# Kernel optimization log

Hardware: AMD Instinct MI355X
Metric: run time of the kernel (lower is better)

The kernel has to match this reference:

```python
import jax, jax.numpy as jnp
import numpy as np

HIS = 10   # history steps (node_feature_dim = 10*4)
ROLL = 2   # args.pred_roll
MP = 2     # message_passing_steps
N = 20000  # num nodes (balls)
E = 320000 # num edges


def _mlp(x, W1, b1, W2, b2, g, be):
    # two-layer ELU MLP + BatchNorm1d (training mode: batch statistics)
    h = jax.nn.elu(x @ W1 + b1)
    h = jax.nn.elu(h @ W2 + b2)
    B, M, C = h.shape
    f = h.reshape(B * M, C)
    mu = f.mean(0)
    var = ((f - mu) ** 2).mean(0)  # biased variance, as torch BN training
    f = (f - mu) * jax.lax.rsqrt(var + 1e-5) * g + be
    return f.reshape(B, M, C)


def setup_inputs() -> dict:
    key = jax.random.key(0)
    ks = jax.random.split(key, 16)

    def lin(k, i, o):
        W = jax.random.normal(k, (i, o), jnp.float32) / jnp.sqrt(jnp.float32(i))
        b = jnp.full((o,), 0.1, jnp.float32)
        return W, b

    inp = {}
    inp["nodes"] = jax.random.normal(ks[0], (1, HIS + ROLL, N, 4), jnp.float32)
    inp["edge_pair"] = jax.random.randint(ks[1], (E, 2), 0, N)
    inp["edge_attr"] = jax.random.normal(ks[2], (E, 2), jnp.float32)
    # encoder node MLP: 40 -> 128 -> 128
    inp["en_W1"], inp["en_b1"] = lin(ks[3], 40, 128)
    inp["en_W2"], inp["en_b2"] = lin(ks[4], 128, 128)
    inp["en_g"], inp["en_be"] = jnp.ones((128,), jnp.float32), jnp.zeros((128,), jnp.float32)
    # encoder edge MLP: 6 -> 32 -> 32
    inp["ee_W1"], inp["ee_b1"] = lin(ks[5], 6, 32)
    inp["ee_W2"], inp["ee_b2"] = lin(ks[6], 32, 32)
    inp["ee_g"], inp["ee_be"] = jnp.ones((32,), jnp.float32), jnp.zeros((32,), jnp.float32)
    # GraphNetBlock edge MLP: 288 -> 128 -> 32
    inp["ge_W1"], inp["ge_b1"] = lin(ks[7], 288, 128)
    inp["ge_W2"], inp["ge_b2"] = lin(ks[8], 128, 32)
    inp["ge_g"], inp["ge_be"] = jnp.ones((32,), jnp.float32), jnp.zeros((32,), jnp.float32)
    # GraphNetBlock node MLP: 160 -> 256 -> 128
    inp["gn_W1"], inp["gn_b1"] = lin(ks[9], 160, 256)
    inp["gn_W2"], inp["gn_b2"] = lin(ks[10], 256, 128)
    inp["gn_g"], inp["gn_be"] = jnp.ones((128,), jnp.float32), jnp.zeros((128,), jnp.float32)
    # decoder: Linear(128,128) Tanh Linear(128,2)
    inp["d_W1"], inp["d_b1"] = lin(ks[11], 128, 128)
    inp["d_W2"], inp["d_b2"] = lin(ks[12], 128, 2)
    return inp


def _forward(nodes, edge_pair, edge_attr,
             en_W1, en_b1, en_W2, en_b2, en_g, en_be,
             ee_W1, ee_b1, ee_W2, ee_b2, ee_g, ee_be,
             ge_W1, ge_b1, ge_W2, ge_b2, ge_g, ge_be,
             gn_W1, gn_b1, gn_W2, gn_b2, gn_g, gn_be,
             d_W1, d_b1, d_W2, d_b2):
    window = nodes[0]                 # [T, N, 4]
    n = window.shape[1]
    s0 = edge_pair[:, 0]
    s1 = edge_pair[:, 1]
    # history features: [1, N, HIS*4]
    history = jnp.transpose(window[:HIS], (1, 0, 2)).reshape(1, n, -1)
    gt_future = window[HIS:]          # [ROLL, N, 4]
    # initial edge features: raw 2-dim attr + |pos/vel diff| (4-dim) -> 6
    pd0 = jnp.abs(window[HIS][s0] - window[HIS][s1])   # [E, 4]
    edge_feat = jnp.concatenate([edge_attr[None], pd0[None]], -1)  # [1, E, 6]
    cur_pos = window[HIS - 1, :, :2]
    cur_vel = window[HIS - 1, :, 2:]
    preds = []
    for _ in range(ROLL):
        ln = _mlp(history, en_W1, en_b1, en_W2, en_b2, en_g, en_be)    # [1,N,128]
        le = _mlp(edge_feat, ee_W1, ee_b1, ee_W2, ee_b2, ee_g, ee_be)  # [1,E,32]
        for _ in range(MP):
            # edge update: gather sender/receiver, MLP
            ef = jnp.concatenate([ln[:, s0], ln[:, s1], le], -1)       # [1,E,288]
            ne = _mlp(ef, ge_W1, ge_b1, ge_W2, ge_b2, ge_g, ge_be)     # [1,E,32]
            # node aggregation: scatter-add at both endpoints
            agg = jnp.zeros((n, ne.shape[-1]), ne.dtype)
            agg = agg.at[s0].add(ne[0]).at[s1].add(ne[0])
            nf = jnp.concatenate([ln, agg[None]], -1)                  # [1,N,160]
            nn_ = _mlp(nf, gn_W1, gn_b1, gn_W2, gn_b2, gn_g, gn_be)
            ln = nn_ + ln
            le = ne + le
        accel = jnp.tanh(ln @ d_W1 + d_b1) @ d_W2 + d_b2               # [1,N,2]
        prev_pos = cur_pos
        cur_pos = 2 * cur_pos + accel - prev_pos                       # [1,N,2]
        cur_vel = cur_vel + accel
        pd = jnp.abs(cur_pos[:, s0] - cur_pos[:, s1])                  # [1,E,2]
        edge_feat = edge_feat.at[:, :, -2:].set(pd)
        preds.append(cur_pos)
        hist4 = history.reshape(1, n, HIS, 4)
        new_state = jnp.concatenate([cur_pos.reshape(1, n, 1, 2),
                                     cur_vel.reshape(1, n, 1, 2)], -1)
        history = jnp.concatenate([hist4[:, :, 1:, :], new_state], -2).reshape(1, n, -1)
    preds = jnp.stack(preds, 1)                                        # [1,ROLL,N,2]
    diff = preds[0] - gt_future[:, :, :2]
    variance = 5e-5
    loss_nll = (diff ** 2 / (2 * variance)).sum() / (ROLL * n)
    loss_mse = (diff ** 2).mean()
    return preds, loss_nll, loss_mse, gt_future


def reference(nodes, edge_pair, edge_attr,
              en_W1, en_b1, en_W2, en_b2, en_g, en_be,
              ee_W1, ee_b1, ee_W2, ee_b2, ee_g, ee_be,
              ge_W1, ge_b1, ge_W2, ge_b2, ge_g, ge_be,
              gn_W1, gn_b1, gn_W2, gn_b2, gn_g, gn_be,
              d_W1, d_b1, d_W2, d_b2):
    return _forward(nodes, edge_pair, edge_attr,
                    en_W1, en_b1, en_W2, en_b2, en_g, en_be,
                    ee_W1, ee_b1, ee_W2, ee_b2, ee_g, ee_be,
                    ge_W1, ge_b1, ge_W2, ge_b2, ge_g, ge_be,
                    gn_W1, gn_b1, gn_W2, gn_b2, gn_g, gn_be,
                    d_W1, d_b1, d_W2, d_b2)
```

## Files before the change

kernel.cpp:

```cpp
#include <hip/hip_runtime.h>


constexpr int NN = 20000;
constexpr int NE = 320000;
constexpr int NSLOT = 32;
constexpr int SSTR = 512;

typedef __attribute__((ext_vector_type(8))) short short8;
typedef __attribute__((ext_vector_type(4))) float f32x4;

__device__ __forceinline__ float act_elu(float x) { return x > 0.f ? x : __expf(x) - 1.f; }
__device__ __forceinline__ unsigned short f2bf(float f) {
  unsigned u = __builtin_bit_cast(unsigned, f);
  return (unsigned short)((u + 0x7FFFu + ((u >> 16) & 1u)) >> 16);
}
__device__ __forceinline__ float bf2f(unsigned short h) {
  unsigned u = ((unsigned)h) << 16; return __builtin_bit_cast(float, u);
}
__device__ __forceinline__ void atomic_pk_bf16(unsigned short* addr, float a, float b) {
  unsigned v = (unsigned)f2bf(a) | ((unsigned)f2bf(b) << 16);
  asm volatile("global_atomic_pk_add_bf16 %0, %1, off"
               :: "v"(addr), "v"(v) : "memory");
}

template<int K1, int K1P, int C1, int C2, int BM, int NWM, int NWC, int NWM2, int NWC2,
         int ACT2, bool STATS, int MODE>
__global__ __launch_bounds__(256) void mlp2_k(
    const unsigned short* __restrict__ A,
    const unsigned short* __restrict__ Wt1, const float* __restrict__ b1,
    const unsigned short* __restrict__ Wt2, const float* __restrict__ b2,
    unsigned short* __restrict__ out, int M, float* __restrict__ stat,
    unsigned short* __restrict__ aggB, const float* __restrict__ statP, float invE,
    const float* __restrict__ gg, const float* __restrict__ gb,
    float* __restrict__ sclW, const int* __restrict__ dg0, const int* __restrict__ dg1)
{
  constexpr int FM  = BM / (16 * NWM);
  constexpr int FC  = C1 / (16 * NWC);
  constexpr int FM2 = BM / (16 * NWM2);
  constexpr int FC2 = C2 / (16 * NWC2);
  constexpr int NKS1 = K1P / 32;
  constexpr int NKS2 = C1 / 32;
  constexpr int AST = K1P + 8;
  constexpr int P1 = C1 + 8;
  constexpr int P2 = C2 + 8;
  constexpr int ACH = K1P / 8;
  static_assert(NWM * NWC == 4 && NWM2 * NWC2 == 4, "4 waves");
  static_assert(C2 <= C1, "repack reuses H1");

  __shared__ unsigned short As[BM * AST];
  __shared__ unsigned short H1[BM * P1];
  __shared__ float red[2][C2];
  __shared__ float s_scl[(MODE == 4) ? 32 : 1], s_shf[(MODE == 4) ? 32 : 1];

  const int tid = threadIdx.x;
  const int row0 = blockIdx.x * BM;
  const int wave = tid >> 6, lane = tid & 63;
  const int wm = wave % NWM, wc = wave / NWM;
  const int wm2 = wave % NWM2, wc2 = wave / NWM2;
  const int lr = lane & 15, kg = lane >> 4;

  if (STATS) for (int i = tid; i < 2 * C2; i += 256) ((float*)red)[i] = 0.f;

  if constexpr (MODE == 4) {
    if (tid < 32) {
      float su = 0.f, sq = 0.f;
      for (int s = 0; s < NSLOT; ++s) {
        su += statP[(size_t)s * SSTR + tid];
        sq += statP[(size_t)s * SSTR + 256 + tid];
      }
      float mu = su * invE;
      float var = sq * invE - mu * mu;
      float sc = rsqrtf(var + 1e-5f) * gg[tid];
      float sh = gb[tid] - mu * sc;
      s_scl[tid] = sc; s_shf[tid] = sh;
      if (blockIdx.x == 0) { sclW[tid] = sc; sclW[32 + tid] = sh; }
    }
    __syncthreads();
  }

  for (int idx = tid; idx < BM * ACH; idx += 256) {
    int m = idx / ACH, chk = idx % ACH;
    int kglob = chk * 8;
    int row = row0 + m;
    uint4 v = make_uint4(0, 0, 0, 0);
    if (row < M) {
      if constexpr (MODE == 0) {
        if (kglob + 8 <= K1) v = *(const uint4*)(A + (size_t)row * K1 + kglob);
      } else if constexpr (MODE == 3) {
        if (chk == 0) v = *(const uint4*)(A + (size_t)row * 8);
      } else {
        if (kglob < 128) {
          v = *(const uint4*)(A + (size_t)row * 128 + kglob);
        } else {
          int c0 = kglob - 128;
          unsigned short* ap = &aggB[(size_t)row * 32 + c0];
          uint4 av4 = *(uint4*)ap;
          *(uint4*)ap = make_uint4(0, 0, 0, 0);
          const unsigned short* avp = (const unsigned short*)&av4;
          float d = (float)(dg0[row] + dg1[row]);
          unsigned short* vp = (unsigned short*)&v;
#pragma unroll
          for (int j = 0; j < 8; ++j)
            vp[j] = f2bf(fmaf(s_scl[c0 + j], bf2f(avp[j]), d * s_shf[c0 + j]));
        }
      }
    }
    *(uint4*)&As[m * AST + chk * 8] = v;
  }
  __syncthreads();

  f32x4 acc1[FM][FC];
#pragma unroll
  for (int i = 0; i < FM; ++i)
#pragma unroll
    for (int j = 0; j < FC; ++j) acc1[i][j] = (f32x4){0.f, 0.f, 0.f, 0.f};

#pragma unroll
  for (int ks = 0; ks < NKS1; ++ks) {
    const int k0 = ks * 32;
    short8 af[FM], bfr[FC];
#pragma unroll
    for (int i = 0; i < FM; ++i) {
      int r = (wm * FM + i) * 16 + lr;
      af[i] = __builtin_bit_cast(short8, *(const uint4*)&As[r * AST + k0 + kg * 8]);
    }
#pragma unroll
    for (int j = 0; j < FC; ++j) {
      int c = (wc * FC + j) * 16 + lr;
      bfr[j] = __builtin_bit_cast(short8, *(const uint4*)&Wt1[(size_t)c * K1P + k0 + kg * 8]);
    }
#pragma unroll
    for (int i = 0; i < FM; ++i)
#pragma unroll
      for (int j = 0; j < FC; ++j)
        acc1[i][j] = __builtin_amdgcn_mfma_f32_16x16x32_bf16(af[i], bfr[j], acc1[i][j], 0, 0, 0);
  }

  {
    float bl1[FC];
#pragma unroll
    for (int j = 0; j < FC; ++j) bl1[j] = b1[(wc * FC + j) * 16 + lr];
#pragma unroll
    for (int i = 0; i < FM; ++i)
#pragma unroll
      for (int t = 0; t < 4; ++t) {
        int rl = (wm * FM + i) * 16 + kg * 4 + t;
#pragma unroll
        for (int j = 0; j < FC; ++j)
          H1[rl * P1 + (wc * FC + j) * 16 + lr] = f2bf(act_elu(acc1[i][j][t] + bl1[j]));
      }
  }
  __syncthreads();

  f32x4 acc2[FM2][FC2];
#pragma unroll
  for (int i = 0; i < FM2; ++i)
#pragma unroll
    for (int j = 0; j < FC2; ++j) acc2[i][j] = (f32x4){0.f, 0.f, 0.f, 0.f};

#pragma unroll
  for (int ks = 0; ks < NKS2; ++ks) {
    const int k0 = ks * 32;
    short8 af[FM2], bfr[FC2];
#pragma unroll
    for (int i = 0; i < FM2; ++i) {
      int r = (wm2 * FM2 + i) * 16 + lr;
      af[i] = __builtin_bit_cast(short8, *(const uint4*)&H1[r * P1 + k0 + kg * 8]);
    }
#pragma unroll
    for (int j = 0; j < FC2; ++j) {
      int c = (wc2 * FC2 + j) * 16 + lr;
      bfr[j] = __builtin_bit_cast(short8, *(const uint4*)&Wt2[(size_t)c * C1 + k0 + kg * 8]);
    }
#pragma unroll
    for (int i = 0; i < FM2; ++i)
#pragma unroll
      for (int j = 0; j < FC2; ++j)
        acc2[i][j] = __builtin_amdgcn_mfma_f32_16x16x32_bf16(af[i], bfr[j], acc2[i][j], 0, 0, 0);
  }
  __syncthreads();

  float psum[FC2], psq[FC2], bl2[FC2];
#pragma unroll
  for (int j = 0; j < FC2; ++j) {
    psum[j] = 0.f; psq[j] = 0.f;
    bl2[j] = b2[(wc2 * FC2 + j) * 16 + lr];
  }
#pragma unroll
  for (int i = 0; i < FM2; ++i)
#pragma unroll
    for (int t = 0; t < 4; ++t) {
      int rl = (wm2 * FM2 + i) * 16 + kg * 4 + t;
      bool ok = (row0 + rl) < M;
#pragma unroll
      for (int j = 0; j < FC2; ++j) {
        float v = acc2[i][j][t] + bl2[j];
        if (ACT2 == 1) v = act_elu(v);
        else if (ACT2 == 2) v = tanhf(v);
        if (STATS && ok) { psum[j] += v; psq[j] += v * v; }
        H1[rl * P2 + (wc2 * FC2 + j) * 16 + lr] = f2bf(v);
      }
    }
  if (STATS) {
#pragma unroll
    for (int j = 0; j < FC2; ++j) {
      int c = (wc2 * FC2 + j) * 16 + lr;
      atomicAdd(&red[0][c], psum[j]);
      atomicAdd(&red[1][c], psq[j]);
    }
  }
  __syncthreads();
  for (int idx = tid; idx < BM * (C2 / 8); idx += 256) {
    int r = idx / (C2 / 8), cc = idx % (C2 / 8);
    int row = row0 + r;
    if (row < M)
      *(uint4*)&out[(size_t)row * C2 + cc * 8] = *(const uint4*)&H1[r * P2 + cc * 8];
  }
  if (STATS) {
    float* st = stat + (size_t)(blockIdx.x & (NSLOT - 1)) * SSTR;
    for (int i = tid; i < C2; i += 256) {
      atomicAdd(&st[i], red[0][i]);
      atomicAdd(&st[256 + i], red[1][i]);
    }
  }
}

template<int K, int C, int BM, int NWM, int NWC, int ACT, int DEC, int BNST>
__global__ __launch_bounds__(256) void mgemm_k(
    const unsigned short* __restrict__ Ah2,
    unsigned short* __restrict__ Aln,
    const unsigned short* __restrict__ Wt, const float* __restrict__ bias,
    unsigned short* __restrict__ out, int M,
    const float* __restrict__ statP, float invN,
    const float* __restrict__ gv, const float* __restrict__ bev,
    const float* __restrict__ pubStat, const float* __restrict__ pubG,
    const float* __restrict__ pubBe, float invPub, float* __restrict__ pubW,
    const float* __restrict__ W2f, const float* __restrict__ b2f,
    float* __restrict__ pos, float* __restrict__ vel, float* __restrict__ preds)
{
  constexpr int FM = BM / (16 * NWM);
  constexpr int FC = C / (16 * NWC);
  constexpr int NKS = K / 32;
  constexpr int AST = K + 8;
  constexpr int P2 = C + 8;
  constexpr int ACH = K / 8;
  static_assert(NWM * NWC == 4, "4 waves");
  static_assert(BNST == 0 || K == 128, "BN staging assumes K=128");

  __shared__ unsigned short As[BM * AST];
  __shared__ unsigned short Ob[BM * P2];
  __shared__ float Wl[DEC ? 256 : 1];
  __shared__ float s_scl[BNST ? 128 : 1], s_shf[BNST ? 128 : 1];

  const int tid = threadIdx.x;
  const int row0 = blockIdx.x * BM;
  const int wave = tid >> 6, lane = tid & 63;
  const int wm = wave % NWM, wc = wave / NWM;
  const int lr = lane & 15, kg = lane >> 4;

  if constexpr (BNST > 0) {
    if (tid < 128) {
      float su = 0.f, sq = 0.f;
      for (int s = 0; s < NSLOT; ++s) {
        su += statP[(size_t)s * SSTR + tid];
        sq += statP[(size_t)s * SSTR + 256 + tid];
      }
      float mu = su * invN;
      float var = sq * invN - mu * mu;
      float sc = rsqrtf(var + 1e-5f) * gv[tid];
      s_scl[tid] = sc; s_shf[tid] = bev[tid] - mu * sc;
    }
    if constexpr (BNST == 1) {
      if (blockIdx.x == 0 && tid >= 128 && tid < 160) {
        int c = tid - 128;
        float su = 0.f, sq = 0.f;
        for (int s = 0; s < NSLOT; ++s) {
          su += pubStat[(size_t)s * SSTR + c];
          sq += pubStat[(size_t)s * SSTR + 256 + c];
        }
        float mu = su * invPub;
        float var = sq * invPub - mu * mu;
        float sc = rsqrtf(var + 1e-5f) * pubG[c];
        pubW[c] = sc; pubW[32 + c] = pubBe[c] - mu * sc;
      }
    }
    __syncthreads();
  }

  for (int idx = tid; idx < BM * ACH; idx += 256) {
    int m = idx / ACH, chk = idx % ACH;
    int kglob = chk * 8;
    int row = row0 + m;
    uint4 v = make_uint4(0, 0, 0, 0);
    if (row < M) {
      if constexpr (BNST == 0) {
        v = *(const uint4*)(Ah2 + (size_t)row * K + kglob);
      } else {
        uint4 h = *(const uint4*)(Ah2 + (size_t)row * 128 + kglob);
        const unsigned short* hp = (const unsigned short*)&h;
        float f[8];
#pragma unroll
        for (int j = 0; j < 8; ++j)
          f[j] = fmaf(bf2f(hp[j]), s_scl[kglob + j], s_shf[kglob + j]);
        if constexpr (BNST >= 2) {
          uint4 l = *(const uint4*)(Aln + (size_t)row * 128 + kglob);
          const unsigned short* lp = (const unsigned short*)&l;
#pragma unroll
          for (int j = 0; j < 8; ++j) f[j] += bf2f(lp[j]);
        }
        unsigned short* vp = (unsigned short*)&v;
#pragma unroll
        for (int j = 0; j < 8; ++j) vp[j] = f2bf(f[j]);
        if constexpr (BNST <= 2)
          *(uint4*)(Aln + (size_t)row * 128 + kglob) = v;
      }
    }
    *(uint4*)&As[m * AST + chk * 8] = v;
  }
  __syncthreads();

  f32x4 acc[FM][FC];
#pragma unroll
  for (int i = 0; i < FM; ++i)
#pragma unroll
    for (int j = 0; j < FC; ++j) acc[i][j] = (f32x4){0.f, 0.f, 0.f, 0.f};

#pragma unroll
  for (int ks = 0; ks < NKS; ++ks) {
    const int k0 = ks * 32;
    short8 af[FM], bfr[FC];
#pragma unroll
    for (int i = 0; i < FM; ++i) {
      int r = (wm * FM + i) * 16 + lr;
      af[i] = __builtin_bit_cast(short8, *(const uint4*)&As[r * AST + k0 + kg * 8]);
    }
#pragma unroll
    for (int j = 0; j < FC; ++j) {
      int c = (wc * FC + j) * 16 + lr;
      bfr[j] = __builtin_bit_cast(short8, *(const uint4*)&Wt[(size_t)c * K + k0 + kg * 8]);
    }
#pragma unroll
    for (int i = 0; i < FM; ++i)
#pragma unroll
      for (int j = 0; j < FC; ++j)
        acc[i][j] = __builtin_amdgcn_mfma_f32_16x16x32_bf16(af[i], bfr[j], acc[i][j], 0, 0, 0);
  }

  float bl[FC];
#pragma unroll
  for (int j = 0; j < FC; ++j) bl[j] = bias[(wc * FC + j) * 16 + lr];
#pragma unroll
  for (int i = 0; i < FM; ++i)
#pragma unroll
    for (int t = 0; t < 4; ++t) {
      int rl = (wm * FM + i) * 16 + kg * 4 + t;
#pragma unroll
      for (int j = 0; j < FC; ++j) {
        float v = acc[i][j][t] + bl[j];
        if (ACT == 1) v = act_elu(v);
        else if (ACT == 2) v = tanhf(v);
        Ob[rl * P2 + (wc * FC + j) * 16 + lr] = f2bf(v);
      }
    }
  if constexpr (DEC) Wl[tid] = W2f[tid];
  __syncthreads();
  if constexpr (DEC) {
    int rloc = tid >> 3, j = tid & 7;
    int row = row0 + rloc;
    float ax = 0.f, ay = 0.f;
#pragma unroll
    for (int kk = 0; kk < 16; ++kk) {
      int k = j + 8 * kk;
      float f = bf2f(Ob[rloc * P2 + k]);
      ax = fmaf(f, Wl[2 * k], ax);
      ay = fmaf(f, Wl[2 * k + 1], ay);
    }
    ax += __shfl_down(ax, 4, 8); ax += __shfl_down(ax, 2, 8); ax += __shfl_down(ax, 1, 8);
    ay += __shfl_down(ay, 4, 8); ay += __shfl_down(ay, 2, 8); ay += __shfl_down(ay, 1, 8);
    if (j == 0 && row < M) {
      float axx = ax + b2f[0], ayy = ay + b2f[1];
      float2 p = ((float2*)pos)[row], vv = ((float2*)vel)[row];
      p.x += axx; p.y += ayy; vv.x += axx; vv.y += ayy;
      ((float2*)pos)[row] = p; ((float2*)vel)[row] = vv;
      ((float2*)preds)[row] = p;
    }
  } else {
    for (int idx = tid; idx < BM * (C / 8); idx += 256) {
      int r = idx / (C / 8), cc = idx % (C / 8);
      int row = row0 + r;
      if (row < M)
        *(uint4*)&out[(size_t)row * C + cc * 8] = *(const uint4*)&Ob[r * P2 + cc * 8];
    }
  }
}

template<int LE, int WOUT>
__global__ __launch_bounds__(256) void ge_edge_k(
    const unsigned short* __restrict__ Pb,
    const unsigned short* __restrict__ e32ee,
    const unsigned short* __restrict__ e32ge,
    const float* __restrict__ sclEE,
    const float* __restrict__ sclGE,
    const int* __restrict__ epP,
    const unsigned short* __restrict__ Wt1c,
    const float* __restrict__ b1,
    const unsigned short* __restrict__ Wt2,
    const float* __restrict__ b2,
    unsigned short* __restrict__ out,
    unsigned short* __restrict__ aggB,
    float* __restrict__ stat)
{
  constexpr int BM = 64;
  constexpr int P1 = 136;
  __shared__ unsigned short Ps[BM * P1];
  __shared__ unsigned short As[BM * 40];
  __shared__ float red[2][32];
  __shared__ int eps[BM * 2];

  const int tid = threadIdx.x;
  const int e0 = blockIdx.x * BM;
  const int wave = tid >> 6, lane = tid & 63;
  const int lr = lane & 15, kg = lane >> 4;
  const int wm = wave & 1, wc = wave >> 1;

  uint4 g0[4], g1[4];
  int gm[4], gch[4];
#pragma unroll
  for (int t = 0; t < 4; ++t) {
    int idx = tid + 256 * t;
    int m = idx >> 4, ch = idx & 15;
    gm[t] = m; gch[t] = ch;
    int s0 = epP[2 * (e0 + m)];
    int s1 = epP[2 * (e0 + m) + 1];
    g0[t] = *(const uint4*)&Pb[(size_t)s0 * 256 + ch * 8];
    g1[t] = *(const uint4*)&Pb[(size_t)s1 * 256 + 128 + ch * 8];
  }

  if (tid < BM * 2) eps[tid] = epP[e0 * 2 + tid];
  {
    int m = tid >> 2, chk = tid & 3;
    size_t base = (size_t)(e0 + m) * 32 + chk * 8;
    uint4 ev = *(const uint4*)&e32ee[base];
    const unsigned short* epv = (const unsigned short*)&ev;
    uint4 ov;
    unsigned short* op = (unsigned short*)&ov;
    if constexpr (LE == 2) {
      uint4 gv2 = *(const uint4*)&e32ge[base];
      const unsigned short* gp = (const unsigned short*)&gv2;
#pragma unroll
      for (int j = 0; j < 8; ++j) {
        int c = chk * 8 + j;
        float le = fmaf(sclEE[c], bf2f(epv[j]), sclEE[32 + c])
                 + fmaf(sclGE[c], bf2f(gp[j]), sclGE[32 + c]);
        op[j] = f2bf(le);
      }
    } else {
#pragma unroll
      for (int j = 0; j < 8; ++j) {
        int c = chk * 8 + j;
        op[j] = f2bf(fmaf(sclEE[c], bf2f(epv[j]), sclEE[32 + c]));
      }
    }
    *(uint4*)&As[m * 40 + chk * 8] = ov;
  }
  short8 wf1[4];
#pragma unroll
  for (int j = 0; j < 4; ++j)
    wf1[j] = __builtin_bit_cast(short8, *(const uint4*)&Wt1c[(size_t)((wc * 4 + j) * 16 + lr) * 32 + kg * 8]);
  if (tid < 64) ((float*)red)[tid] = 0.f;
  __syncthreads();

  f32x4 acc1[2][4];
#pragma unroll
  for (int i = 0; i < 2; ++i)
#pragma unroll
    for (int j = 0; j < 4; ++j) acc1[i][j] = (f32x4){0.f, 0.f, 0.f, 0.f};
  {
    short8 af[2];
#pragma unroll
    for (int i = 0; i < 2; ++i)
      af[i] = __builtin_bit_cast(short8, *(const uint4*)&As[((wm * 2 + i) * 16 + lr) * 40 + kg * 8]);
#pragma unroll
    for (int i = 0; i < 2; ++i)
#pragma unroll
      for (int j = 0; j < 4; ++j)
        acc1[i][j] = __builtin_amdgcn_mfma_f32_16x16x32_bf16(af[i], wf1[j], acc1[i][j], 0, 0, 0);
  }

#pragma unroll
  for (int t = 0; t < 4; ++t) {
    uint4 o;
    const unsigned short* ap = (const unsigned short*)&g0[t];
    const unsigned short* bp = (const unsigned short*)&g1[t];
    unsigned short* op = (unsigned short*)&o;
#pragma unroll
    for (int j = 0; j < 8; ++j) op[j] = f2bf(bf2f(ap[j]) + bf2f(bp[j]));
    *(uint4*)&Ps[gm[t] * P1 + gch[t] * 8] = o;
  }
  __syncthreads();

  {
    float bl1[4];
#pragma unroll
    for (int j = 0; j < 4; ++j) bl1[j] = b1[(wc * 4 + j) * 16 + lr];
#pragma unroll
    for (int i = 0; i < 2; ++i)
#pragma unroll
      for (int t = 0; t < 4; ++t) {
        int rl = (wm * 2 + i) * 16 + kg * 4 + t;
#pragma unroll
        for (int j = 0; j < 4; ++j) {
          int a = rl * P1 + (wc * 4 + j) * 16 + lr;
          Ps[a] = f2bf(act_elu(acc1[i][j][t] + bl1[j] + bf2f(Ps[a])));
        }
      }
  }
  __syncthreads();

  f32x4 acc2[2];
  acc2[0] = (f32x4){0.f, 0.f, 0.f, 0.f};
  acc2[1] = (f32x4){0.f, 0.f, 0.f, 0.f};
  const int r2 = wave * 16 + lr;
#pragma unroll
  for (int ks = 0; ks < 4; ++ks) {
    int k0 = ks * 32;
    short8 a2 = __builtin_bit_cast(short8, *(const uint4*)&Ps[r2 * P1 + k0 + kg * 8]);
#pragma unroll
    for (int j = 0; j < 2; ++j) {
      short8 b2v = __builtin_bit_cast(short8, *(const uint4*)&Wt2[(size_t)(j * 16 + lr) * 128 + k0 + kg * 8]);
      acc2[j] = __builtin_amdgcn_mfma_f32_16x16x32_bf16(a2, b2v, acc2[j], 0, 0, 0);
    }
  }

  float psum[2] = {0.f, 0.f}, psq[2] = {0.f, 0.f};
  float bl2[2] = {b2[lr], b2[16 + lr]};
#pragma unroll
  for (int t = 0; t < 4; ++t) {
    int rl = wave * 16 + kg * 4 + t;
#pragma unroll
    for (int j = 0; j < 2; ++j) {
      float v = act_elu(acc2[j][t] + bl2[j]);
      psum[j] += v; psq[j] += v * v;
      As[rl * 40 + j * 16 + lr] = f2bf(v);
    }
  }
#pragma unroll
  for (int j = 0; j < 2; ++j) {
    atomicAdd(&red[0][j * 16 + lr], psum[j]);
    atomicAdd(&red[1][j * 16 + lr], psq[j]);
  }
  __syncthreads();
  if (WOUT) {
    int m = tid >> 2, chk = tid & 3;
    *(uint4*)&out[(size_t)(e0 + m) * 32 + chk * 8] = *(const uint4*)&As[m * 40 + chk * 8];
  }
  {
    int cp = tid & 15;
    int gsel = tid >> 4;
    int rbeg = gsel * 4;
    float a0 = 0.f, a1 = 0.f;
    int cur = eps[2 * rbeg];
#pragma unroll
    for (int r = 0; r < 4; ++r) {
      int row = rbeg + r;
      unsigned pv = *(const unsigned*)&As[row * 40 + 2 * cp];
      float v0 = bf2f((unsigned short)(pv & 0xFFFF));
      float v1 = bf2f((unsigned short)(pv >> 16));
      int s0 = eps[2 * row];
      if (s0 != cur) {
        atomic_pk_bf16(&aggB[(size_t)cur * 32 + 2 * cp], a0, a1);
        a0 = 0.f; a1 = 0.f; cur = s0;
      }
      a0 += v0; a1 += v1;
      atomic_pk_bf16(&aggB[(size_t)eps[2 * row + 1] * 32 + 2 * cp], v0, v1);
    }
    atomic_pk_bf16(&aggB[(size_t)cur * 32 + 2 * cp], a0, a1);
  }
  if (tid < 32) {
    float* st = stat + (size_t)(blockIdx.x & (NSLOT - 1)) * SSTR;
    atomicAdd(&st[tid], red[0][tid]);
    atomicAdd(&st[256 + tid], red[1][tid]);
  }
}

__global__ __launch_bounds__(256) void wtrans_all_k(
    const float* __restrict__ enW1, const float* __restrict__ enW2,
    const float* __restrict__ geW1, const float* __restrict__ geW2,
    const float* __restrict__ gnW1, const float* __restrict__ gnW2,
    const float* __restrict__ dW1,  const float* __restrict__ eeW1,
    const float* __restrict__ eeW2,
    unsigned short* __restrict__ enW1t, unsigned short* __restrict__ enW2t,
    unsigned short* __restrict__ gePt,  unsigned short* __restrict__ geCt,
    unsigned short* __restrict__ geW2t,
    unsigned short* __restrict__ gnW1t, unsigned short* __restrict__ gnW2t,
    unsigned short* __restrict__ dW1t,  unsigned short* __restrict__ eeW1t,
    unsigned short* __restrict__ eeW2t)
{
  int i = blockIdx.x * 256 + threadIdx.x;
#define SEG(Wsrc, Wdst, NROW, SRCS, KS, KP) \
  { int n = (NROW) * (KP); \
    if (i < n) { int c = i / (KP), k = i - c * (KP); \
      (Wdst)[i] = (k < (KS)) ? f2bf((Wsrc)[(size_t)k * (SRCS) + c]) : (unsigned short)0; return; } \
    i -= n; }
  SEG(enW1, enW1t, 128, 128, 40, 64)
  SEG(enW2, enW2t, 128, 128, 128, 128)
  SEG(geW1, gePt, 128, 128, 128, 128)
  SEG(geW1 + 128 * 128, gePt + 128 * 128, 128, 128, 128, 128)
  SEG(geW1 + 256 * 128, geCt, 128, 128, 32, 32)
  SEG(geW2, geW2t, 32, 32, 128, 128)
  SEG(gnW1, gnW1t, 256, 256, 160, 160)
  SEG(gnW2, gnW2t, 128, 128, 256, 256)
  SEG(dW1,  dW1t,  128, 128, 128, 128)
  SEG(eeW1, eeW1t, 32, 32, 6, 32)
  SEG(eeW2, eeW2t, 32, 32, 32, 32)
#undef SEG
}
constexpr int WT_TOTAL = 128*64 + 128*128 + 128*128 + 128*128 + 128*32 + 32*128
                       + 256*160 + 128*256 + 128*128 + 32*32 + 32*32;

__global__ __launch_bounds__(256) void csr_count0_k(const int* __restrict__ ep,
    int* __restrict__ deg0, int E)
{
  int e = blockIdx.x * 256 + threadIdx.x;
  if (e < E) atomicAdd(&deg0[ep[2 * e]], 1);
}

__global__ __launch_bounds__(1024) void csr_scan_k(const int* __restrict__ deg,
    int* __restrict__ off, int* __restrict__ cursor, int N)
{
  __shared__ int part[1024];
  int t = threadIdx.x;
  const int CHK = (N + 1023) / 1024;
  int c0 = t * CHK, c1 = min(c0 + CHK, N);
  int s = 0;
  for (int i = c0; i < c1; ++i) s += deg[i];
  part[t] = s;
  __syncthreads();
  for (int o = 1; o < 1024; o <<= 1) {
    int v = (t >= o) ? part[t - o] : 0;
    __syncthreads();
    part[t] += v;
    __syncthreads();
  }
  int run = t ? part[t - 1] : 0;
  for (int i = c0; i < c1; ++i) { int d = deg[i]; off[i] = run; cursor[i] = run; run += d; }
}

__global__ __launch_bounds__(256) void csr_fill0_k(const int* __restrict__ ep,
    int* __restrict__ cursor0, int* __restrict__ perm, int E)
{
  int e = blockIdx.x * 256 + threadIdx.x;
  if (e < E) { int p = atomicAdd(&cursor0[ep[2 * e]], 1); perm[p] = e; }
}

__global__ __launch_bounds__(256) void permute_edges_k(const float4* __restrict__ nodes4,
    const float* __restrict__ attr, const int* __restrict__ ep,
    const int* __restrict__ perm, int* __restrict__ epP,
    unsigned short* __restrict__ efb, int* __restrict__ deg1, int E)
{
  int e2 = blockIdx.x * 256 + threadIdx.x;
  if (e2 >= E) return;
  int e = perm[e2];
  int s0 = ep[2 * e], s1 = ep[2 * e + 1];
  epP[2 * e2] = s0; epP[2 * e2 + 1] = s1;
  atomicAdd(&deg1[s1], 1);
  float4 w0 = nodes4[(size_t)10 * NN + s0];
  float4 w1 = nodes4[(size_t)10 * NN + s1];
  float2 a = ((const float2*)attr)[e];
  uint4 o;
  o.x = (unsigned)f2bf(a.x) | ((unsigned)f2bf(a.y) << 16);
  o.y = (unsigned)f2bf(fabsf(w0.x - w1.x)) | ((unsigned)f2bf(fabsf(w0.y - w1.y)) << 16);
  o.z = (unsigned)f2bf(fabsf(w0.z - w1.z)) | ((unsigned)f2bf(fabsf(w0.w - w1.w)) << 16);
  o.w = 0;
  ((uint4*)efb)[e2] = o;
}

__global__ __launch_bounds__(256) void pd_upd_k(const float* __restrict__ pos,
    const int* __restrict__ epP, unsigned short* __restrict__ efb, int E)
{
  int e = blockIdx.x * 256 + threadIdx.x;
  if (e >= E) return;
  float2 p0 = ((const float2*)pos)[epP[2 * e]];
  float2 p1 = ((const float2*)pos)[epP[2 * e + 1]];
  unsigned u = (unsigned)f2bf(fabsf(p0.x - p1.x)) | ((unsigned)f2bf(fabsf(p0.y - p1.y)) << 16);
  *(unsigned*)&efb[(size_t)e * 8 + 4] = u;
}

__global__ __launch_bounds__(256) void hist_shift_k(float* __restrict__ hist,
    unsigned short* __restrict__ histb,
    const float* __restrict__ pos, const float* __restrict__ vel, int M)
{
  int n = blockIdx.x * 256 + threadIdx.x;
  if (n >= M) return;
  float4* h4 = (float4*)(hist + (size_t)n * 40);
  float4 tmp[10];
#pragma unroll
  for (int t = 0; t < 10; ++t) tmp[t] = h4[t];
  float2 pp = ((const float2*)pos)[n], vv = ((const float2*)vel)[n];
  unsigned* hb = (unsigned*)(histb + (size_t)n * 40);
#pragma unroll
  for (int t = 0; t < 9; ++t) {
    float4 v = tmp[t + 1];
    h4[t] = v;
    hb[2 * t]     = (unsigned)f2bf(v.x) | ((unsigned)f2bf(v.y) << 16);
    hb[2 * t + 1] = (unsigned)f2bf(v.z) | ((unsigned)f2bf(v.w) << 16);
  }
  float4 nv = make_float4(pp.x, pp.y, vv.x, vv.y);
  h4[9] = nv;
  hb[18] = (unsigned)f2bf(nv.x) | ((unsigned)f2bf(nv.y) << 16);
  hb[19] = (unsigned)f2bf(nv.z) | ((unsigned)f2bf(nv.w) << 16);
}

__global__ __launch_bounds__(256) void init_nodes_k(const float4* __restrict__ nodes4,
    float* __restrict__ hist, unsigned short* __restrict__ histb,
    float* __restrict__ pos, float* __restrict__ vel,
    float* __restrict__ outGt, int M)
{
  int n = blockIdx.x * 256 + threadIdx.x;
  if (n >= M) return;
  float4* h4 = (float4*)(hist + (size_t)n * 40);
  unsigned* hb = (unsigned*)(histb + (size_t)n * 40);
  float4 v;
#pragma unroll
  for (int t = 0; t < 10; ++t) {
    v = nodes4[(size_t)t * M + n];
    h4[t] = v;
    hb[2 * t]     = (unsigned)f2bf(v.x) | ((unsigned)f2bf(v.y) << 16);
    hb[2 * t + 1] = (unsigned)f2bf(v.z) | ((unsigned)f2bf(v.w) << 16);
  }
  ((float2*)pos)[n] = make_float2(v.x, v.y);
  ((float2*)vel)[n] = make_float2(v.z, v.w);
  float4 g0 = nodes4[(size_t)10 * M + n];
  float4 g1 = nodes4[(size_t)11 * M + n];
  float2* gt2 = (float2*)outGt;
  gt2[(size_t)2 * n + 0] = make_float2(g0.x, g0.y);
  gt2[(size_t)2 * n + 1] = make_float2(g0.z, g0.w);
  gt2[(size_t)2 * (M + n) + 0] = make_float2(g1.x, g1.y);
  gt2[(size_t)2 * (M + n) + 1] = make_float2(g1.z, g1.w);
}

__global__ __launch_bounds__(256) void loss_k(const float* __restrict__ preds,
    const float* __restrict__ gtf, float* __restrict__ acc)
{
  int i = blockIdx.x * 256 + threadIdx.x;
  float d2 = 0.f;
  if (i < 2 * NN * 2) {
    int r = i / (NN * 2);
    int rem = i - r * (NN * 2);
    int n = rem >> 1, c = rem & 1;
    float df = preds[i] - gtf[((size_t)r * NN + n) * 4 + c];
    d2 = df * df;
  }
#pragma unroll
  for (int o = 32; o > 0; o >>= 1) d2 += __shfl_down(d2, o, 64);
  __shared__ float sb[4];
  int lane = threadIdx.x & 63, w = threadIdx.x >> 6;
  if (lane == 0) sb[w] = d2;
  __syncthreads();
  if (threadIdx.x == 0) atomicAdd(acc, sb[0] + sb[1] + sb[2] + sb[3]);
}

__global__ void loss_write_k(const float* __restrict__ acc, float* __restrict__ o)
{
  float s = *acc;
  o[0] = s * 0.25f;
  o[1] = s * (1.f / 80000.f);
}

extern "C" void kernel_launch(void* const* d_in, const int* in_sizes, int n_in,
                              void* d_out, int out_size, void* d_ws, size_t ws_size,
                              hipStream_t stream)
{
  (void)in_sizes; (void)n_in; (void)out_size; (void)ws_size;
  const float* nodes = (const float*)d_in[0];
  const int*   ep    = (const int*)d_in[1];
  const float* eattr = (const float*)d_in[2];
  const float *en_W1 = (const float*)d_in[3],  *en_b1 = (const float*)d_in[4],
              *en_W2 = (const float*)d_in[5],  *en_b2 = (const float*)d_in[6],
              *en_g  = (const float*)d_in[7],  *en_be = (const float*)d_in[8];
  const float *ee_W1 = (const float*)d_in[9],  *ee_b1 = (const float*)d_in[10],
              *ee_W2 = (const float*)d_in[11], *ee_b2 = (const float*)d_in[12],
              *ee_g  = (const float*)d_in[13], *ee_be = (const float*)d_in[14];
  const float *ge_W1 = (const float*)d_in[15], *ge_b1 = (const float*)d_in[16],
              *ge_W2 = (const float*)d_in[17], *ge_b2 = (const float*)d_in[18],
              *ge_g  = (const float*)d_in[19], *ge_be = (const float*)d_in[20];
  const float *gn_W1 = (const float*)d_in[21], *gn_b1 = (const float*)d_in[22],
              *gn_W2 = (const float*)d_in[23], *gn_b2 = (const float*)d_in[24],
              *gn_g  = (const float*)d_in[25], *gn_be = (const float*)d_in[26];
  const float *d_W1  = (const float*)d_in[27], *d_b1  = (const float*)d_in[28],
              *d_W2  = (const float*)d_in[29], *d_b2  = (const float*)d_in[30];

  float* out = (float*)d_out;
  float* outPreds = out;
  float* outLoss  = out + 80000;
  float* outGt    = out + 80002;

  float* ws = (float*)d_ws;
  size_t off = 0;
  auto alloc = [&](size_t nf) { float* p = ws + off; off += (nf + 15) & ~(size_t)15; return p; };
  float* hist  = alloc((size_t)NN * 40);
  unsigned short* histb = (unsigned short*)alloc((size_t)NN * 20);
  unsigned short* efb   = (unsigned short*)alloc((size_t)NE * 4);
  unsigned short* lnb  = (unsigned short*)alloc((size_t)NN * 64);
  unsigned short* e32ee = (unsigned short*)alloc((size_t)NE * 16);
  unsigned short* e32ge = (unsigned short*)alloc((size_t)NE * 16);
  unsigned short* Pb   = (unsigned short*)alloc((size_t)NN * 128);
  unsigned short* h2nb = (unsigned short*)alloc((size_t)NN * 64);
  unsigned short* aggB = (unsigned short*)alloc((size_t)NN * 16);
  float* pos   = alloc((size_t)NN * 2);
  float* vel   = alloc((size_t)NN * 2);
  unsigned short* enW1t = (unsigned short*)alloc(128 * 64 / 2);
  unsigned short* enW2t = (unsigned short*)alloc(128 * 128 / 2);
  unsigned short* gePt  = (unsigned short*)alloc(256 * 128 / 2);
  unsigned short* geCt  = (unsigned short*)alloc(128 * 32 / 2);
  unsigned short* geW2t = (unsigned short*)alloc(32 * 128 / 2);
  unsigned short* gnW1t = (unsigned short*)alloc(256 * 160 / 2);
  unsigned short* gnW2t = (unsigned short*)alloc(128 * 256 / 2);
  unsigned short* dW1t  = (unsigned short*)alloc(128 * 128 / 2);
  unsigned short* eeW1t = (unsigned short*)alloc(32 * 32 / 2);
  unsigned short* eeW2t = (unsigned short*)alloc(32 * 32 / 2);
  const size_t SLOTSZ = (size_t)NSLOT * SSTR;
  float* statArr = alloc(12 * SLOTSZ + 256 + 16);
  float* zerosF  = statArr + 12 * SLOTSZ;
  float* lacc    = zerosF + 256;
  float* sclshfEE = alloc(64);
  float* sclshfGE = alloc(64);
  int* deg0    = (int*)alloc(NN);
  int* off0    = (int*)alloc(NN);
  int* cursor0 = (int*)alloc(NN);
  int* deg1    = (int*)alloc(NN);
  int* perm    = (int*)alloc(NE);
  int* epP     = (int*)alloc(2 * (size_t)NE);

  hipMemsetAsync(statArr, 0, (12 * SLOTSZ + 256 + 16) * sizeof(float), stream);
  hipMemsetAsync(deg0, 0, NN * sizeof(int), stream);
  hipMemsetAsync(deg1, 0, NN * sizeof(int), stream);
  hipMemsetAsync(aggB, 0, (size_t)NN * 32 * sizeof(unsigned short), stream);

  wtrans_all_k<<<(WT_TOTAL + 255) / 256, 256, 0, stream>>>(
      en_W1, en_W2, ge_W1, ge_W2, gn_W1, gn_W2, d_W1, ee_W1, ee_W2,
      enW1t, enW2t, gePt, geCt, geW2t, gnW1t, gnW2t, dW1t, eeW1t, eeW2t);

  init_nodes_k<<<(NN + 255) / 256, 256, 0, stream>>>((const float4*)nodes, hist, histb, pos, vel, outGt, NN);

  csr_count0_k<<<(NE + 255) / 256, 256, 0, stream>>>(ep, deg0, NE);
  csr_scan_k<<<1, 1024, 0, stream>>>(deg0, off0, cursor0, NN);
  csr_fill0_k<<<(NE + 255) / 256, 256, 0, stream>>>(ep, cursor0, perm, NE);
  permute_edges_k<<<(NE + 255) / 256, 256, 0, stream>>>(
      (const float4*)nodes, eattr, ep, perm, epP, efb, deg1, NE);

  const int GN32 = (NN + 31) / 32;
  const int GE128 = NE / 128;
  const int GE64 = NE / 64;
  const float invE = 1.f / NE;
  const float invN = 1.f / NN;

  for (int r = 0; r < 2; ++r) {
    float* sEN  = statArr + (size_t)(r * 6 + 0) * SLOTSZ;
    float* sEE  = statArr + (size_t)(r * 6 + 1) * SLOTSZ;
    float* sGE0 = statArr + (size_t)(r * 6 + 2) * SLOTSZ;
    float* sGN0 = statArr + (size_t)(r * 6 + 3) * SLOTSZ;
    float* sGE1 = statArr + (size_t)(r * 6 + 4) * SLOTSZ;
    float* sGN1 = statArr + (size_t)(r * 6 + 5) * SLOTSZ;

    mlp2_k<40, 64, 128, 128, 32, 2, 2, 2, 2, 1, true, 0><<<GN32, 256, 0, stream>>>(
        histb, enW1t, en_b1, enW2t, en_b2, h2nb, NN, sEN,
        nullptr, nullptr, 0.f, nullptr, nullptr, nullptr, nullptr, nullptr);
    mlp2_k<32, 32, 32, 32, 128, 4, 1, 4, 1, 1, true, 3><<<GE128, 256, 0, stream>>>(
        efb, eeW1t, ee_b1, eeW2t, ee_b2, e32ee, NE, sEE,
        nullptr, nullptr, 0.f, nullptr, nullptr, nullptr, nullptr, nullptr);

    mgemm_k<128, 256, 32, 2, 2, 0, 0, 1><<<GN32, 256, 0, stream>>>(
        h2nb, lnb, gePt, zerosF, Pb, NN,
        sEN, invN, en_g, en_be,
        sEE, ee_g, ee_be, invE, sclshfEE,
        nullptr, nullptr, nullptr, nullptr, nullptr);
    ge_edge_k<1, 1><<<GE64, 256, 0, stream>>>(Pb, e32ee, nullptr, sclshfEE, nullptr,
        epP, geCt, ge_b1, geW2t, ge_b2, e32ge, aggB, sGE0);
    mlp2_k<160, 160, 256, 128, 32, 2, 2, 2, 2, 1, true, 4><<<GN32, 256, 0, stream>>>(
        lnb, gnW1t, gn_b1, gnW2t, gn_b2, h2nb, NN, sGN0,
        aggB, sGE0, invE, ge_g, ge_be, sclshfGE, deg0, deg1);

    mgemm_k<128, 256, 32, 2, 2, 0, 0, 2><<<GN32, 256, 0, stream>>>(
        h2nb, lnb, gePt, zerosF, Pb, NN,
        sGN0, invN, gn_g, gn_be,
        nullptr, nullptr, nullptr, 0.f, nullptr,
        nullptr, nullptr, nullptr, nullptr, nullptr);
    ge_edge_k<2, 0><<<GE64, 256, 0, stream>>>(Pb, e32ee, e32ge, sclshfEE, sclshfGE,
        epP, geCt, ge_b1, geW2t, ge_b2, nullptr, aggB, sGE1);
    mlp2_k<160, 160, 256, 128, 32, 2, 2, 2, 2, 1, true, 4><<<GN32, 256, 0, stream>>>(
        lnb, gnW1t, gn_b1, gnW2t, gn_b2, h2nb, NN, sGN1,
        aggB, sGE1, invE, ge_g, ge_be, sclshfGE, deg0, deg1);

    mgemm_k<128, 128, 32, 2, 2, 2, 1, 3><<<GN32, 256, 0, stream>>>(
        h2nb, lnb, dW1t, d_b1, nullptr, NN,
        sGN1, invN, gn_g, gn_be,
        nullptr, nullptr, nullptr, 0.f, nullptr,
        d_W2, d_b2, pos, vel, outPreds + (size_t)r * NN * 2);

    if (r == 0) {
      pd_upd_k<<<(NE + 255) / 256, 256, 0, stream>>>(pos, epP, efb, NE);
      hist_shift_k<<<(NN + 255) / 256, 256, 0, stream>>>(hist, histb, pos, vel, NN);
    }
  }

  loss_k<<<(2 * NN * 2 + 255) / 256, 256, 0, stream>>>(outPreds, outGt, lacc);
  loss_write_k<<<1, 1, 0, stream>>>(lacc, outLoss);
}
```

Before: 715.6 us.

## Replace receiver-side bf16 atomics with CSR gather in node MLP

Edge kernels no longer scatter per-edge atomics to the second endpoint. Instead they always write per-edge outputs, and the node MLP gathers those rows through a new second CSR (off1/eidx1) built once at setup. This is meant to remove heavy random atomic traffic, including bf16 rounding from many atomic adds. In exchange it adds an extra edge-output write in the second block (reusing the e32ee buffer) and serial per-row gather loops whose length depends on node degree, which may cause divergence.

Measured after the change: 906.2 us. +26.6%, slower.

```diff
diff --git a/kernel.cpp b/kernel.cpp
--- a/kernel.cpp
+++ b/kernel.cpp
@@ -32,7 +32,9 @@
     unsigned short* __restrict__ out, int M, float* __restrict__ stat,
     unsigned short* __restrict__ aggB, const float* __restrict__ statP, float invE,
     const float* __restrict__ gg, const float* __restrict__ gb,
-    float* __restrict__ sclW, const int* __restrict__ dg0, const int* __restrict__ dg1)
+    float* __restrict__ sclW, const int* __restrict__ dg0, const int* __restrict__ dg1,
+    const unsigned short* __restrict__ h2e, const int* __restrict__ off1,
+    const int* __restrict__ eidx1)
 {
   constexpr int FM  = BM / (16 * NWM);
   constexpr int FC  = C1 / (16 * NWC);
@@ -97,11 +99,22 @@
           uint4 av4 = *(uint4*)ap;
           *(uint4*)ap = make_uint4(0, 0, 0, 0);
           const unsigned short* avp = (const unsigned short*)&av4;
-          float d = (float)(dg0[row] + dg1[row]);
+          float acc[8];
+#pragma unroll
+          for (int j = 0; j < 8; ++j) acc[j] = bf2f(avp[j]);
+          int o1 = off1[row], d1v = dg1[row];
+          for (int i = 0; i < d1v; ++i) {
+            int e = eidx1[o1 + i];
+            uint4 hv = *(const uint4*)&h2e[(size_t)e * 32 + c0];
+            const unsigned short* hp = (const unsigned short*)&hv;
+#pragma unroll
+            for (int j = 0; j < 8; ++j) acc[j] += bf2f(hp[j]);
+          }
+          float d = (float)(dg0[row] + d1v);
           unsigned short* vp = (unsigned short*)&v;
 #pragma unroll
           for (int j = 0; j < 8; ++j)
-            vp[j] = f2bf(fmaf(s_scl[c0 + j], bf2f(avp[j]), d * s_shf[c0 + j]));
+            vp[j] = f2bf(fmaf(s_scl[c0 + j], acc[j], d * s_shf[c0 + j]));
         }
       }
     }
@@ -394,7 +407,7 @@
   }
 }
 
-template<int LE, int WOUT>
+template<int LE>
 __global__ __launch_bounds__(256) void ge_edge_k(
     const unsigned short* __restrict__ Pb,
     const unsigned short* __restrict__ e32ee,
@@ -550,7 +563,7 @@
     atomicAdd(&red[1][j * 16 + lr], psq[j]);
   }
   __syncthreads();
-  if (WOUT) {
+  {
     int m = tid >> 2, chk = tid & 3;
     *(uint4*)&out[(size_t)(e0 + m) * 32 + chk * 8] = *(const uint4*)&As[m * 40 + chk * 8];
   }
@@ -572,7 +585,6 @@
         a0 = 0.f; a1 = 0.f; cur = s0;
       }
       a0 += v0; a1 += v1;
-      atomic_pk_bf16(&aggB[(size_t)eps[2 * row + 1] * 32 + 2 * cp], v0, v1);
     }
     atomic_pk_bf16(&aggB[(size_t)cur * 32 + 2 * cp], a0, a1);
   }
@@ -673,6 +685,13 @@
   o.z = (unsigned)f2bf(fabsf(w0.z - w1.z)) | ((unsigned)f2bf(fabsf(w0.w - w1.w)) << 16);
   o.w = 0;
   ((uint4*)efb)[e2] = o;
+}
+
+__global__ __launch_bounds__(256) void csr_fill1_k(const int* __restrict__ epP,
+    int* __restrict__ cursor1, int* __restrict__ eidx1, int E)
+{
+  int e = blockIdx.x * 256 + threadIdx.x;
+  if (e < E) { int p = atomicAdd(&cursor1[epP[2 * e + 1]], 1); eidx1[p] = e; }
 }
 
 __global__ __launch_bounds__(256) void pd_upd_k(const float* __restrict__ pos,
@@ -829,8 +848,11 @@
   int* off0    = (int*)alloc(NN);
   int* cursor0 = (int*)alloc(NN);
   int* deg1    = (int*)alloc(NN);
+  int* off1    = (int*)alloc(NN);
+  int* cursor1 = (int*)alloc(NN);
   int* perm    = (int*)alloc(NE);
   int* epP     = (int*)alloc(2 * (size_t)NE);
+  int* eidx1   = (int*)alloc(NE);
 
   hipMemsetAsync(statArr, 0, (12 * SLOTSZ + 256 + 16) * sizeof(float), stream);
   hipMemsetAsync(deg0, 0, NN * sizeof(int), stream);
@@ -848,6 +870,8 @@
   csr_fill0_k<<<(NE + 255) / 256, 256, 0, stream>>>(ep, cursor0, perm, NE);
   permute_edges_k<<<(NE + 255) / 256, 256, 0, stream>>>(
       (const float4*)nodes, eattr, ep, perm, epP, efb, deg1, NE);
+  csr_scan_k<<<1, 1024, 0, stream>>>(deg1, off1, cursor1, NN);
+  csr_fill1_k<<<(NE + 255) / 256, 256, 0, stream>>>(epP, cursor1, eidx1, NE);
 
   const int GN32 = (NN + 31) / 32;
   const int GE128 = NE / 128;
@@ -865,32 +889,36 @@
 
     mlp2_k<40, 64, 128, 128, 32, 2, 2, 2, 2, 1, true, 0><<<GN32, 256, 0, stream>>>(
         histb, enW1t, en_b1, enW2t, en_b2, h2nb, NN, sEN,
-        nullptr, nullptr, 0.f, nullptr, nullptr, nullptr, nullptr, nullptr);
+        nullptr, nullptr, 0.f, nullptr, nullptr, nullptr, nullptr, nullptr,
+        nullptr, nullptr, nullptr);
     mlp2_k<32, 32, 32, 32, 128, 4, 1, 4, 1, 1, true, 3><<<GE128, 256, 0, stream>>>(
         efb, eeW1t, ee_b1, eeW2t, ee_b2, e32ee, NE, sEE,
-        nullptr, nullptr, 0.f, nullptr, nullptr, nullptr, nullptr, nullptr);
+        nullptr, nullptr, 0.f, nullptr, nullptr, nullptr, nullptr, nullptr,
+        nullptr, nullptr, nullptr);
 
     mgemm_k<128, 256, 32, 2, 2, 0, 0, 1><<<GN32, 256, 0, stream>>>(
         h2nb, lnb, gePt, zerosF, Pb, NN,
         sEN, invN, en_g, en_be,
         sEE, ee_g, ee_be, invE, sclshfEE,
         nullptr, nullptr, nullptr, nullptr, nullptr);
-    ge_edge_k<1, 1><<<GE64, 256, 0, stream>>>(Pb, e32ee, nullptr, sclshfEE, nullptr,
+    ge_edge_k<1><<<GE64, 256, 0, stream>>>(Pb, e32ee, nullptr, sclshfEE, nullptr,
         epP, geCt, ge_b1, geW2t, ge_b2, e32ge, aggB, sGE0);
     mlp2_k<160, 160, 256, 128, 32, 2, 2, 2, 2, 1, true, 4><<<GN32, 256, 0, stream>>>(
         lnb, gnW1t, gn_b1, gnW2t, gn_b2, h2nb, NN, sGN0,
-        aggB, sGE0, invE, ge_g, ge_be, sclshfGE, deg0, deg1);
+        aggB, sGE0, invE, ge_g, ge_be, sclshfGE, deg0, deg1,
+        e32ge, off1, eidx1);
 
     mgemm_k<128, 256, 32, 2, 2, 0, 0, 2><<<GN32, 256, 0, stream>>>(
         h2nb, lnb, gePt, zerosF, Pb, NN,
         sGN0, invN, gn_g, gn_be,
         nullptr, nullptr, nullptr, 0.f, nullptr,
         nullptr, nullptr, nullptr, nullptr, nullptr);
-    ge_edge_k<2, 0><<<GE64, 256, 0, stream>>>(Pb, e32ee, e32ge, sclshfEE, sclshfGE,
-        epP, geCt, ge_b1, geW2t, ge_b2, nullptr, aggB, sGE1);
+    ge_edge_k<2><<<GE64, 256, 0, stream>>>(Pb, e32ee, e32ge, sclshfEE, sclshfGE,
+        epP, geCt, ge_b1, geW2t, ge_b2, e32ee, aggB, sGE1);
     mlp2_k<160, 160, 256, 128, 32, 2, 2, 2, 2, 1, true, 4><<<GN32, 256, 0, stream>>>(
         lnb, gnW1t, gn_b1, gnW2t, gn_b2, h2nb, NN, sGN1,
-        aggB, sGE1, invE, ge_g, ge_be, sclshfGE, deg0, deg1);
+        aggB, sGE1, invE, ge_g, ge_be, sclshfGE, deg0, deg1,
+        e32ee, off1, eidx1);
 
     mgemm_k<128, 128, 32, 2, 2, 2, 1, 3><<<GN32, 256, 0, stream>>>(
         h2nb, lnb, dW1t, d_b1, nullptr, NN,
```
